# Performance work log

Measured on AMD Instinct MI355X. Metric: run time of the kernel, lower is better.

Reference implementation:

```python
import jax, jax.numpy as jnp
import numpy as np

N_NODES = 50000
N_EDGES = 800000


def setup_inputs() -> dict:
    key = jax.random.key(0)
    ks = jax.random.split(key, 8)
    return {
        "x": jax.random.normal(ks[0], (N_NODES, 256), dtype=jnp.float32),
        "adj_vals": jax.random.uniform(ks[1], (N_EDGES,), dtype=jnp.float32),
        "rows": jax.random.randint(ks[2], (N_EDGES,), 0, N_NODES, dtype=jnp.int32),
        "cols": jax.random.randint(ks[3], (N_EDGES,), 0, N_NODES, dtype=jnp.int32),
        "W1": jax.random.normal(ks[4], (256, 256), dtype=jnp.float32) * (1.0 / np.sqrt(256)),
        "b1": jnp.zeros((256,), dtype=jnp.float32),
        "W2": jax.random.normal(ks[5], (256, 256), dtype=jnp.float32) * (1.0 / np.sqrt(256)),
        "b2": jnp.zeros((256,), dtype=jnp.float32),
        "W3": jax.random.normal(ks[6], (256, 128), dtype=jnp.float32) * (1.0 / np.sqrt(256)),
        "b3": jnp.zeros((128,), dtype=jnp.float32),
    }


def reference(x, adj_vals, rows, cols, W1, b1, W2, b2, W3, b3):
    n = x.shape[0]

    def spmm(h):
        # sparse adjacency matmul: out[r] += val * h[c] over all edges (r, c)
        return jax.ops.segment_sum(adj_vals[:, None] * h[cols], rows, num_segments=n)

    # GCNLayer: adj @ (x @ W) + b ; ReLU between layers (dropout p=0 => identity)
    h = jax.nn.relu(spmm(x @ W1) + b1)
    h = jax.nn.relu(spmm(h @ W2) + b2)
    return spmm(h @ W3) + b3
```

## Files before the change

kernel.cpp:

```cpp
#include <hip/hip_runtime.h>
#include <hip/hip_bf16.h>


#define N_NODES 50000
#define N_EDGES 800000
#define KDIM 256
#define REP 16
#define NC (N_NODES * REP)
#define NB2 ((NC + 1023) / 1024)
#define NC_PAD (NB2 * 1024)

#define PB_CAST 6250
#define PB_HIST 782
#define PB_TR   640

typedef __attribute__((ext_vector_type(8))) short short8;
typedef __attribute__((ext_vector_type(4))) float f32x4;

__device__ __forceinline__ ushort f2bf(float f) {
    union { float f; unsigned u; } x; x.f = f;
    unsigned r = x.u + 0x7fffu + ((x.u >> 16) & 1u);
    return (ushort)(r >> 16);
}
__device__ __forceinline__ float bf2f(ushort u) {
    union { unsigned u; float f; } x; x.u = ((unsigned)u) << 16;
    return x.f;
}

__global__ __launch_bounds__(256) void prep_kernel(
        const float* __restrict__ x, ushort* __restrict__ xb,
        const int* __restrict__ rows, int* __restrict__ counts,
        const float* __restrict__ W1, const float* __restrict__ W2,
        const float* __restrict__ W3, ushort* __restrict__ Wt1,
        ushort* __restrict__ Wt2, ushort* __restrict__ Wt3) {
    int b = blockIdx.x, t = threadIdx.x;
    if (b < PB_CAST) {
        int i = (b * 256 + t) * 8;
        float4 f0 = *(const float4*)&x[i];
        float4 f1 = *(const float4*)&x[i + 4];
        short8 o;
        o[0] = (short)f2bf(f0.x); o[1] = (short)f2bf(f0.y);
        o[2] = (short)f2bf(f0.z); o[3] = (short)f2bf(f0.w);
        o[4] = (short)f2bf(f1.x); o[5] = (short)f2bf(f1.y);
        o[6] = (short)f2bf(f1.z); o[7] = (short)f2bf(f1.w);
        *(short8*)&xb[i] = o;
    } else if (b < PB_CAST + PB_HIST) {
        int e0 = (b - PB_CAST) * 1024 + t * 4;
        if (e0 + 3 < N_EDGES) {
            int4 r4 = *(const int4*)&rows[e0];
            atomicAdd(&counts[(r4.x << 4) | ((e0    ) & 15)], 1);
            atomicAdd(&counts[(r4.y << 4) | ((e0 + 1) & 15)], 1);
            atomicAdd(&counts[(r4.z << 4) | ((e0 + 2) & 15)], 1);
            atomicAdd(&counts[(r4.w << 4) | ((e0 + 3) & 15)], 1);
        } else {
            for (int j = 0; j < 4; j++) {
                int e = e0 + j;
                if (e < N_EDGES) atomicAdd(&counts[(rows[e] << 4) | (e & 15)], 1);
            }
        }
    } else {
        int id = (b - PB_CAST - PB_HIST) * 256 + t;
        if (id < 65536) {
            int n = id >> 8, k = id & 255;
            Wt1[n * 256 + k] = f2bf(W1[k * 256 + n]);
        } else if (id < 131072) {
            int i = id - 65536, n = i >> 8, k = i & 255;
            Wt2[n * 256 + k] = f2bf(W2[k * 256 + n]);
        } else {
            int i = id - 131072, n = i >> 8, k = i & 255;
            Wt3[n * 256 + k] = f2bf(W3[k * 128 + n]);
        }
    }
}


__global__ __launch_bounds__(256) void scan_sums(const int* __restrict__ counts,
                                                 int* __restrict__ bsum) {
    __shared__ int ws[4];
    int b = blockIdx.x, t = threadIdx.x, lane = t & 63, wv = t >> 6;
    int4 v = *(const int4*)&counts[b * 1024 + t * 4];
    int s = v.x + v.y + v.z + v.w;
    #pragma unroll
    for (int off = 32; off >= 1; off >>= 1) s += __shfl_down(s, off, 64);
    if (lane == 0) ws[wv] = s;
    __syncthreads();
    if (t == 0) bsum[b] = ws[0] + ws[1] + ws[2] + ws[3];
}

__global__ __launch_bounds__(1024) void scan_block(const int* __restrict__ bsum,
                                                   int* __restrict__ boff,
                                                   int* __restrict__ rp16, int nb) {
    __shared__ int ws[16];
    int t = threadIdx.x, lane = t & 63, wv = t >> 6;
    int v = (t < nb) ? bsum[t] : 0;
    int incl = v;
    #pragma unroll
    for (int off = 1; off < 64; off <<= 1) {
        int u = __shfl_up(incl, off, 64);
        if (lane >= off) incl += u;
    }
    if (lane == 63) ws[wv] = incl;
    __syncthreads();
    int wo = 0;
    #pragma unroll
    for (int j = 0; j < 15; j++) wo += (j < wv) ? ws[j] : 0;
    if (t < nb) boff[t] = wo + incl - v;
    if (t == 1023) rp16[NC] = wo + incl;
}

__global__ __launch_bounds__(256) void scan_apply(int* __restrict__ counts,
                                                  const int* __restrict__ boff,
                                                  int* __restrict__ rp16) {
    __shared__ int ws[4];
    int b = blockIdx.x, t = threadIdx.x, lane = t & 63, wv = t >> 6;
    int i = b * 1024 + t * 4;
    int4 v = *(const int4*)&counts[i];
    int s0 = v.x, s01 = s0 + v.y, s012 = s01 + v.z, tsum = s012 + v.w;
    int incl = tsum;
    #pragma unroll
    for (int off = 1; off < 64; off <<= 1) {
        int u = __shfl_up(incl, off, 64);
        if (lane >= off) incl += u;
    }
    if (lane == 63) ws[wv] = incl;
    __syncthreads();
    int woff = 0;
    #pragma unroll
    for (int j = 0; j < 3; j++) woff += (j < wv) ? ws[j] : 0;
    int base = boff[b] + woff + incl - tsum;
    if (i < NC)     rp16[i]     = base;
    if (i + 1 < NC) rp16[i + 1] = base + s0;
    if (i + 2 < NC) rp16[i + 2] = base + s01;
    if (i + 3 < NC) rp16[i + 3] = base + s012;
    *(int4*)&counts[i] = make_int4(0, 0, 0, 0);
}

__global__ void scatter_kernel(const int* __restrict__ rows, const int* __restrict__ cols,
                               const float* __restrict__ vals, const int* __restrict__ rp16,
                               int* __restrict__ counts, int2* __restrict__ cv) {
    int e = blockIdx.x * blockDim.x + threadIdx.x;
    if (e < N_EDGES) {
        int idx = (rows[e] << 4) | (e & 15);
        int pos = rp16[idx] + atomicAdd(&counts[idx], 1);
        cv[pos] = make_int2(cols[e], __float_as_int(vals[e]));
    }
}


__global__ __launch_bounds__(256) void gemm_kernel(
        const ushort* __restrict__ A, const ushort* __restrict__ Wt,
        ushort* __restrict__ C, int M, int N) {
    __shared__ ushort Ws[128 * 256];

    int t = threadIdx.x, lane = t & 63, w = t >> 6;
    int row0 = blockIdx.x * 256 + w * 64;
    int col0 = blockIdx.y * 128;
    int q = lane >> 4, mi = lane & 15;

    #pragma unroll
    for (int i = 0; i < 16; i++) {
        int u = i * 256 + t;
        int c = u >> 5, ch = u & 31;
        *(short8*)&Ws[c * 256 + (ch ^ (c & 31)) * 8] =
            *(const short8*)&Wt[(col0 + c) * KDIM + ch * 8];
    }
    __syncthreads();

    f32x4 acc[4][8];
    #pragma unroll
    for (int i = 0; i < 4; i++)
        #pragma unroll
        for (int j = 0; j < 8; j++) acc[i][j] = (f32x4)0.f;

    #pragma unroll
    for (int ks = 0; ks < 8; ks++) {
        int kc = ks * 4 + q;
        short8 af[4], bf[8];
        #pragma unroll
        for (int mt = 0; mt < 4; mt++) {
            int gr = row0 + mt * 16 + mi;
            if (gr >= M) gr = M - 1;
            af[mt] = *(const short8*)&A[gr * KDIM + kc * 8];
        }
        #pragma unroll
        for (int nt = 0; nt < 8; nt++) {
            int cc = nt * 16 + mi;
            bf[nt] = *(const short8*)&Ws[cc * 256 + (kc ^ (cc & 31)) * 8];
        }
        #pragma unroll
        for (int mt = 0; mt < 4; mt++)
            #pragma unroll
            for (int nt = 0; nt < 8; nt++)
                acc[mt][nt] = __builtin_amdgcn_mfma_f32_16x16x32_bf16(
                    af[mt], bf[nt], acc[mt][nt], 0, 0, 0);
    }

    #pragma unroll
    for (int mt = 0; mt < 4; mt++) {
        #pragma unroll
        for (int r = 0; r < 4; r++) {
            int grow = row0 + mt * 16 + q * 4 + r;
            if (grow < M) {
                #pragma unroll
                for (int nt = 0; nt < 8; nt++)
                    C[grow * N + col0 + nt * 16 + mi] = f2bf(acc[mt][nt][r]);
            }
        }
    }
}


template <int F, bool RELU, bool OUT_BF16>
__global__ __launch_bounds__(256) void spmm_kernel(
        const ushort* __restrict__ H, const int* __restrict__ rp16,
        const int2* __restrict__ cv, const float* __restrict__ bias,
        void* __restrict__ out, int nrows) {
    constexpr int FL = F / 8;
    constexpr int EP = 64 / FL;
    constexpr int STEP = EP * 8;
    int wave = threadIdx.x >> 6, lane = threadIdx.x & 63;
    int r = blockIdx.x * 4 + wave;
    if (r >= nrows) return;
    int fl = lane % FL, ep = lane / FL;
    const ushort* Hl = H + fl * 8;

    float acc[8];
    #pragma unroll
    for (int j = 0; j < 8; j++) acc[j] = 0.f;

    int start = rp16[r * REP], end = rp16[r * REP + REP];
    for (int base = start; base < end; base += STEP) {
        int e0 = base + ep * 8;
        int2 m[8];
        #pragma unroll
        for (int i = 0; i < 8; i++) m[i] = cv[e0 + i];
        int c[8]; float v[8];
        #pragma unroll
        for (int i = 0; i < 8; i++) {
            bool p = (e0 + i) < end;
            c[i] = p ? m[i].x : 0;
            v[i] = p ? __int_as_float(m[i].y) : 0.f;
        }
        short8 h[8];
        #pragma unroll
        for (int i = 0; i < 8; i++) h[i] = *(const short8*)&Hl[(size_t)c[i] * F];
        #pragma unroll
        for (int i = 0; i < 8; i++)
            #pragma unroll
            for (int j = 0; j < 8; j++)
                acc[j] += v[i] * bf2f((ushort)h[i][j]);
    }

    #pragma unroll
    for (int off = FL; off < 64; off <<= 1)
        #pragma unroll
        for (int j = 0; j < 8; j++) acc[j] += __shfl_down(acc[j], off, 64);

    if (ep == 0) {
        #pragma unroll
        for (int j = 0; j < 8; j++) {
            float o = acc[j] + bias[fl * 8 + j];
            if (RELU) o = fmaxf(o, 0.f);
            acc[j] = o;
        }
        if (OUT_BF16) {
            short8 ob;
            #pragma unroll
            for (int j = 0; j < 8; j++) ob[j] = (short)f2bf(acc[j]);
            *(short8*)((ushort*)out + (size_t)r * F + fl * 8) = ob;
        } else {
            float* of = (float*)out + (size_t)r * F + fl * 8;
            *(float4*)&of[0] = make_float4(acc[0], acc[1], acc[2], acc[3]);
            *(float4*)&of[4] = make_float4(acc[4], acc[5], acc[6], acc[7]);
        }
    }
}


extern "C" void kernel_launch(void* const* d_in, const int* in_sizes, int n_in,
                              void* d_out, int out_size, void* d_ws, size_t ws_size,
                              hipStream_t stream) {
    const float* x    = (const float*)d_in[0];
    const float* av   = (const float*)d_in[1];
    const int*   rows = (const int*)d_in[2];
    const int*   cols = (const int*)d_in[3];
    const float* W1   = (const float*)d_in[4];
    const float* b1   = (const float*)d_in[5];
    const float* W2   = (const float*)d_in[6];
    const float* b2   = (const float*)d_in[7];
    const float* W3   = (const float*)d_in[8];
    const float* b3   = (const float*)d_in[9];
    float* out = (float*)d_out;

    const int N = N_NODES, E = N_EDGES;

    char* p = (char*)d_ws;
    auto carve = [&](size_t bytes) {
        void* q = (void*)p;
        p += (bytes + 255) & ~(size_t)255;
        return q;
    };
    ushort* xb   = (ushort*)carve((size_t)N * 256 * 2);
    ushort* bufG = (ushort*)carve((size_t)N * 256 * 2);
    ushort* bufH = (ushort*)carve((size_t)N * 256 * 2);
    ushort* Wt1  = (ushort*)carve((size_t)256 * 256 * 2);
    ushort* Wt2  = (ushort*)carve((size_t)256 * 256 * 2);
    ushort* Wt3  = (ushort*)carve((size_t)128 * 256 * 2);
    int*    rp16   = (int*)carve((size_t)(NC + 1) * 4);
    int*    counts = (int*)carve((size_t)NC_PAD * 4);
    int*    bsum   = (int*)carve((size_t)NB2 * 4);
    int*    boff   = (int*)carve((size_t)NB2 * 4);
    int2*   cv     = (int2*)carve((size_t)(E + 64) * 8);

    hipMemsetAsync(counts, 0, (size_t)NC_PAD * 4, stream);
    prep_kernel<<<PB_CAST + PB_HIST + PB_TR, 256, 0, stream>>>(
        x, xb, rows, counts, W1, W2, W3, Wt1, Wt2, Wt3);

    scan_sums<<<NB2, 256, 0, stream>>>(counts, bsum);
    scan_block<<<1, 1024, 0, stream>>>(bsum, boff, rp16, NB2);
    scan_apply<<<NB2, 256, 0, stream>>>(counts, boff, rp16);
    scatter_kernel<<<(E + 255) / 256, 256, 0, stream>>>(rows, cols, av, rp16, counts, cv);

    dim3 g2((N + 255) / 256, 2);
    dim3 g1((N + 255) / 256, 1);
    int spmm_blocks = (N + 3) / 4;

    gemm_kernel<<<g2, 256, 0, stream>>>(xb, Wt1, bufG, N, 256);
    spmm_kernel<256, true, true><<<spmm_blocks, 256, 0, stream>>>(bufG, rp16, cv, b1, bufH, N);
    gemm_kernel<<<g2, 256, 0, stream>>>(bufH, Wt2, bufG, N, 256);
    spmm_kernel<256, true, true><<<spmm_blocks, 256, 0, stream>>>(bufG, rp16, cv, b2, bufH, N);
    gemm_kernel<<<g1, 256, 0, stream>>>(bufH, Wt3, bufG, N, 128);
    spmm_kernel<128, false, false><<<spmm_blocks, 256, 0, stream>>>(bufG, rp16, cv, b3, out, N);
}
```

Baseline: 395.8 us.

## Software-pipeline SpMM edge gathers and split GEMM columns across eight waves

The SpMM inner loop now prefetches the next chunk of edge metadata and feature rows while accumulating the current one, using 4 edges per lane instead of 8. The tail padding of the edge array is zeroed so that the speculative prefetch past the end reads valid column indices. The GEMM moves to 512-thread blocks where each wave covers 64 output columns, halving accumulator registers and raising occupancy. The cost is a wider register live range for the double buffer and duplicated A-tile loads across the two column waves.

```diff
diff --git a/kernel.cpp b/kernel.cpp
--- a/kernel.cpp
+++ b/kernel.cpp
@@ -89,9 +89,11 @@
 
 __global__ __launch_bounds__(1024) void scan_block(const int* __restrict__ bsum,
                                                    int* __restrict__ boff,
-                                                   int* __restrict__ rp16, int nb) {
+                                                   int* __restrict__ rp16,
+                                                   int2* __restrict__ cv_pad, int nb) {
     __shared__ int ws[16];
     int t = threadIdx.x, lane = t & 63, wv = t >> 6;
+    if (t < 64) cv_pad[t] = make_int2(0, 0);
     int v = (t < nb) ? bsum[t] : 0;
     int incl = v;
     #pragma unroll
@@ -147,35 +149,36 @@
 }
 
 
-__global__ __launch_bounds__(256) void gemm_kernel(
+__global__ __launch_bounds__(512, 4) void gemm_kernel(
         const ushort* __restrict__ A, const ushort* __restrict__ Wt,
         ushort* __restrict__ C, int M, int N) {
     __shared__ ushort Ws[128 * 256];
 
     int t = threadIdx.x, lane = t & 63, w = t >> 6;
-    int row0 = blockIdx.x * 256 + w * 64;
-    int col0 = blockIdx.y * 128;
+    int wr = w & 3, wc = w >> 2;
+    int row0 = blockIdx.x * 256 + wr * 64;
+    int colb = blockIdx.y * 128;
     int q = lane >> 4, mi = lane & 15;
 
     #pragma unroll
-    for (int i = 0; i < 16; i++) {
-        int u = i * 256 + t;
+    for (int i = 0; i < 8; i++) {
+        int u = i * 512 + t;
         int c = u >> 5, ch = u & 31;
         *(short8*)&Ws[c * 256 + (ch ^ (c & 31)) * 8] =
-            *(const short8*)&Wt[(col0 + c) * KDIM + ch * 8];
+            *(const short8*)&Wt[(colb + c) * KDIM + ch * 8];
     }
     __syncthreads();
 
-    f32x4 acc[4][8];
+    f32x4 acc[4][4];
     #pragma unroll
     for (int i = 0; i < 4; i++)
         #pragma unroll
-        for (int j = 0; j < 8; j++) acc[i][j] = (f32x4)0.f;
+        for (int j = 0; j < 4; j++) acc[i][j] = (f32x4)0.f;
 
     #pragma unroll
     for (int ks = 0; ks < 8; ks++) {
         int kc = ks * 4 + q;
-        short8 af[4], bf[8];
+        short8 af[4], bf[4];
         #pragma unroll
         for (int mt = 0; mt < 4; mt++) {
             int gr = row0 + mt * 16 + mi;
@@ -183,14 +186,14 @@
             af[mt] = *(const short8*)&A[gr * KDIM + kc * 8];
         }
         #pragma unroll
-        for (int nt = 0; nt < 8; nt++) {
-            int cc = nt * 16 + mi;
+        for (int nt = 0; nt < 4; nt++) {
+            int cc = wc * 64 + nt * 16 + mi;
             bf[nt] = *(const short8*)&Ws[cc * 256 + (kc ^ (cc & 31)) * 8];
         }
         #pragma unroll
         for (int mt = 0; mt < 4; mt++)
             #pragma unroll
-            for (int nt = 0; nt < 8; nt++)
+            for (int nt = 0; nt < 4; nt++)
                 acc[mt][nt] = __builtin_amdgcn_mfma_f32_16x16x32_bf16(
                     af[mt], bf[nt], acc[mt][nt], 0, 0, 0);
     }
@@ -202,8 +205,8 @@
             int grow = row0 + mt * 16 + q * 4 + r;
             if (grow < M) {
                 #pragma unroll
-                for (int nt = 0; nt < 8; nt++)
-                    C[grow * N + col0 + nt * 16 + mi] = f2bf(acc[mt][nt][r]);
+                for (int nt = 0; nt < 4; nt++)
+                    C[grow * N + colb + wc * 64 + nt * 16 + mi] = f2bf(acc[mt][nt][r]);
             }
         }
     }
@@ -217,7 +220,8 @@
         void* __restrict__ out, int nrows) {
     constexpr int FL = F / 8;
     constexpr int EP = 64 / FL;
-    constexpr int STEP = EP * 8;
+    constexpr int D  = 4;
+    constexpr int STEP = EP * D;
     int wave = threadIdx.x >> 6, lane = threadIdx.x & 63;
     int r = blockIdx.x * 4 + wave;
     if (r >= nrows) return;
@@ -229,26 +233,32 @@
     for (int j = 0; j < 8; j++) acc[j] = 0.f;
 
     int start = rp16[r * REP], end = rp16[r * REP + REP];
-    for (int base = start; base < end; base += STEP) {
-        int e0 = base + ep * 8;
-        int2 m[8];
-        #pragma unroll
-        for (int i = 0; i < 8; i++) m[i] = cv[e0 + i];
-        int c[8]; float v[8];
-        #pragma unroll
-        for (int i = 0; i < 8; i++) {
-            bool p = (e0 + i) < end;
-            c[i] = p ? m[i].x : 0;
-            v[i] = p ? __int_as_float(m[i].y) : 0.f;
-        }
-        short8 h[8];
-        #pragma unroll
-        for (int i = 0; i < 8; i++) h[i] = *(const short8*)&Hl[(size_t)c[i] * F];
-        #pragma unroll
-        for (int i = 0; i < 8; i++)
-            #pragma unroll
-            for (int j = 0; j < 8; j++)
-                acc[j] += v[i] * bf2f((ushort)h[i][j]);
+    if (start < end) {
+        int2 mc[D]; short8 hc[D];
+        int e0 = start + ep * D;
+        #pragma unroll
+        for (int i = 0; i < D; i++) mc[i] = cv[e0 + i];
+        #pragma unroll
+        for (int i = 0; i < D; i++) hc[i] = *(const short8*)&Hl[(size_t)mc[i].x * F];
+
+        for (int base = start; base < end; base += STEP) {
+            int en = base + STEP + ep * D;
+            int2 mn[D]; short8 hn[D];
+            #pragma unroll
+            for (int i = 0; i < D; i++) mn[i] = cv[en + i];
+            #pragma unroll
+            for (int i = 0; i < D; i++) hn[i] = *(const short8*)&Hl[(size_t)mn[i].x * F];
+            int ec = base + ep * D;
+            #pragma unroll
+            for (int i = 0; i < D; i++) {
+                float v = (ec + i < end) ? __int_as_float(mc[i].y) : 0.f;
+                #pragma unroll
+                for (int j = 0; j < 8; j++)
+                    acc[j] += v * bf2f((ushort)hc[i][j]);
+            }
+            #pragma unroll
+            for (int i = 0; i < D; i++) { mc[i] = mn[i]; hc[i] = hn[i]; }
+        }
     }
 
     #pragma unroll
@@ -317,7 +327,7 @@
         x, xb, rows, counts, W1, W2, W3, Wt1, Wt2, Wt3);
 
     scan_sums<<<NB2, 256, 0, stream>>>(counts, bsum);
-    scan_block<<<1, 1024, 0, stream>>>(bsum, boff, rp16, NB2);
+    scan_block<<<1, 1024, 0, stream>>>(bsum, boff, rp16, cv + E, NB2);
     scan_apply<<<NB2, 256, 0, stream>>>(counts, boff, rp16);
     scatter_kernel<<<(E + 255) / 256, 256, 0, stream>>>(rows, cols, av, rp16, counts, cv);
 
@@ -325,10 +335,10 @@
     dim3 g1((N + 255) / 256, 1);
     int spmm_blocks = (N + 3) / 4;
 
-    gemm_kernel<<<g2, 256, 0, stream>>>(xb, Wt1, bufG, N, 256);
+    gemm_kernel<<<g2, 512, 0, stream>>>(xb, Wt1, bufG, N, 256);
     spmm_kernel<256, true, true><<<spmm_blocks, 256, 0, stream>>>(bufG, rp16, cv, b1, bufH, N);
-    gemm_kernel<<<g2, 256, 0, stream>>>(bufH, Wt2, bufG, N, 256);
+    gemm_kernel<<<g2, 512, 0, stream>>>(bufH, Wt2, bufG, N, 256);
     spmm_kernel<256, true, true><<<spmm_blocks, 256, 0, stream>>>(bufG, rp16, cv, b2, bufH, N);
-    gemm_kernel<<<g1, 256, 0, stream>>>(bufH, Wt3, bufG, N, 128);
+    gemm_kernel<<<g1, 512, 0, stream>>>(bufH, Wt3, bufG, N, 128);
     spmm_kernel<128, false, false><<<spmm_blocks, 256, 0, stream>>>(bufG, rp16, cv, b3, out, N);
 }
```

After: 429.4 us. 1.08x slower.
